# Performance work log

Measured on AMD Instinct MI355X. Metric: run time of the kernel, lower is better.

Reference implementation:

```python
import jax, jax.numpy as jnp
import numpy as np

N_HEAD = 16

def _rope_cos_sin(T, head_dim, dtype):
    # inv_freq over even indices, freqs [T, head_dim//2]
    inv_freq = 1.0 / (10000.0 ** (jnp.arange(0, head_dim, 2, dtype=jnp.float32) / head_dim))
    t = jnp.arange(T, dtype=jnp.float32)
    freqs = t[:, None] * inv_freq[None, :]
    cos = jnp.cos(freqs).astype(dtype)[None, :, None, :]  # [1,T,1,hd/2]
    sin = jnp.sin(freqs).astype(dtype)[None, :, None, :]
    return cos, sin

def _apply_rope(x, cos, sin):
    # x: [B,T,H,hd]; interleaved halves as in the torch module
    x1, x2 = x[..., ::2], x[..., 1::2]
    return jnp.concatenate([x1 * cos - x2 * sin, x1 * sin + x2 * cos], axis=-1)

def setup_inputs() -> dict:
    key = jax.random.key(0)
    k1, k2, k3 = jax.random.split(key, 3)
    B, T, C = 2, 2048, 1024
    x = jax.random.normal(k1, (B, T, C), dtype=jnp.float32)
    # causal mask (mask==0 positions get -inf), broadcast over B and heads
    attn_mask = jnp.tril(jnp.ones((T, T), dtype=bool))[None, None, :, :]
    w_qkv = jax.random.normal(k2, (C, 3 * C), dtype=jnp.float32) * (1.0 / np.sqrt(C))
    w_out = jax.random.normal(k3, (C, C), dtype=jnp.float32) * (1.0 / np.sqrt(C))
    return {"x": x, "attn_mask": attn_mask, "w_qkv": w_qkv, "w_out": w_out}

def reference(x, attn_mask, w_qkv, w_out):
    B, T, C = x.shape
    H = N_HEAD
    hd = C // H
    qkv = x @ w_qkv  # [B,T,3C]
    q, k, v = jnp.split(qkv, 3, axis=2)
    q = q.reshape(B, T, H, hd)
    k = k.reshape(B, T, H, hd)
    v = v.reshape(B, T, H, hd)
    cos, sin = _rope_cos_sin(T, hd, x.dtype)
    q = _apply_rope(q, cos, sin)
    k = _apply_rope(k, cos, sin)
    scale = 1.0 / np.sqrt(hd).astype(np.float32)
    att = jnp.einsum('bthd,bshd->bhts', q, k) * scale  # [B,H,T,T]
    att = jnp.where(attn_mask, att, -jnp.inf)
    att = jax.nn.softmax(att, axis=-1)
    out = jnp.einsum('bhts,bshd->bthd', att, v).reshape(B, T, C)
    out = out @ w_out
    k_t = jnp.transpose(k, (0, 2, 1, 3))  # [B,H,T,hd]
    v_t = jnp.transpose(v, (0, 2, 1, 3))
    return out, k_t, v_t
```

## Files before the change

kernel.cpp:

```cpp
#include <hip/hip_runtime.h>

#define T_SEQ 2048
#define NH    16
#define HD    64
#define CDIM  1024
#define BDIM  2

using floatx4 = __attribute__((ext_vector_type(4))) float;
using bf16x8  = __attribute__((ext_vector_type(8))) __bf16;
using half4   = __attribute__((ext_vector_type(4))) _Float16;
using half8   = __attribute__((ext_vector_type(8))) _Float16;
typedef unsigned short u16;

__device__ __forceinline__ u16 f2bf(float f) {
  unsigned int u = __float_as_uint(f);
  u += 0x7fffu + ((u >> 16) & 1u);
  return (u16)(u >> 16);
}
__device__ __forceinline__ float bf2f(u16 h) {
  return __uint_as_float(((unsigned int)h) << 16);
}
__device__ __forceinline__ u16 f2h(float f) {
  union { _Float16 h; u16 u; } c; c.h = (_Float16)f; return c.u;
}
__device__ __forceinline__ unsigned pk2h(float a, float b) {
  return __builtin_bit_cast(unsigned, __builtin_amdgcn_cvt_pkrtz(a, b));
}
__device__ __forceinline__ void gld16(const void* g, const void* l) {
  __builtin_amdgcn_global_load_lds(
      (const __attribute__((address_space(1))) unsigned int*)(unsigned long long)g,
      (__attribute__((address_space(3))) unsigned int*)(unsigned int)(unsigned long long)l,
      16, 0, 0);
}

__global__ __launch_bounds__(256) void preproc(const float* __restrict__ x,
                                               const float* __restrict__ w_qkv,
                                               const float* __restrict__ w_out,
                                               u16* __restrict__ xb,
                                               u16* __restrict__ wqT,
                                               u16* __restrict__ woT) {
  __shared__ float tile[32][33];
  int blk = blockIdx.x, tid = threadIdx.x;
  if (blk < 4096) {
    int i = blk * 256 + tid;
    float4 v = ((const float4*)x)[i];
    ushort4 o;
    o.x = f2bf(v.x); o.y = f2bf(v.y); o.z = f2bf(v.z); o.w = f2bf(v.w);
    ((ushort4*)xb)[i] = o;
    return;
  }
  const float* W; u16* WT; int K, N, bx, by;
  if (blk < 4096 + 3072) {
    int idx = blk - 4096; W = w_qkv; WT = wqT; K = 1024; N = 3072;
    bx = idx % 96; by = idx / 96;
  } else {
    int idx = blk - 7168; W = w_out; WT = woT; K = 1024; N = 1024;
    bx = idx & 31; by = idx >> 5;
  }
  int n0 = bx * 32, k0 = by * 32;
  int tx = tid & 31, ty = tid >> 5;
#pragma unroll
  for (int i = 0; i < 32; i += 8)
    tile[ty + i][tx] = W[(size_t)(k0 + ty + i) * N + n0 + tx];
  __syncthreads();
#pragma unroll
  for (int i = 0; i < 32; i += 8)
    WT[(size_t)(n0 + ty + i) * K + k0 + tx] = f2bf(tile[tx][ty + i]);
}

template <bool OUT_F32>
__global__ __launch_bounds__(256) void gemm_bt(const u16* __restrict__ A,
                                               const u16* __restrict__ BT,
                                               float* __restrict__ Cf,
                                               u16* __restrict__ Cb,
                                               int M, int N, int K) {
  __shared__ u16 As[128 * 32];
  __shared__ u16 Bs[128 * 32];
  const int tid  = threadIdx.x;
  const int lane = tid & 63, wave = tid >> 6;
  const int quad = lane >> 4, l16 = lane & 15;
  const int wm = (wave & 1) * 64, wn = (wave >> 1) * 64;
  const int row0 = blockIdx.x * 128, col0 = blockIdx.y * 128;
  const int srow = tid >> 2;
  const int sc   = tid & 3;
  const int sgc  = (sc ^ ((srow >> 1) & 3)) * 8;
  floatx4 acc[4][4] = {};
  for (int k0 = 0; k0 < K; k0 += 32) {
    __syncthreads();
    gld16(A  + (size_t)(row0 + srow     ) * K + k0 + sgc, &As[srow * 32 + sc * 8]);
    gld16(A  + (size_t)(row0 + srow + 64) * K + k0 + sgc, &As[(srow + 64) * 32 + sc * 8]);
    gld16(BT + (size_t)(col0 + srow     ) * K + k0 + sgc, &Bs[srow * 32 + sc * 8]);
    gld16(BT + (size_t)(col0 + srow + 64) * K + k0 + sgc, &Bs[(srow + 64) * 32 + sc * 8]);
    __syncthreads();
    bf16x8 af[4], bfv[4];
#pragma unroll
    for (int mt = 0; mt < 4; mt++) {
      int r = wm + mt * 16 + l16;
      af[mt] = *(const bf16x8*)&As[r * 32 + (quad ^ ((r >> 1) & 3)) * 8];
    }
#pragma unroll
    for (int nt = 0; nt < 4; nt++) {
      int r = wn + nt * 16 + l16;
      bfv[nt] = *(const bf16x8*)&Bs[r * 32 + (quad ^ ((r >> 1) & 3)) * 8];
    }
#pragma unroll
    for (int mt = 0; mt < 4; mt++)
#pragma unroll
      for (int nt = 0; nt < 4; nt++)
        acc[mt][nt] = __builtin_amdgcn_mfma_f32_16x16x32_bf16(af[mt], bfv[nt], acc[mt][nt], 0, 0, 0);
  }
#pragma unroll
  for (int mt = 0; mt < 4; mt++)
#pragma unroll
    for (int nt = 0; nt < 4; nt++)
#pragma unroll
      for (int r = 0; r < 4; r++) {
        int row = row0 + wm + mt * 16 + quad * 4 + r;
        int col = col0 + wn + nt * 16 + l16;
        float v = acc[mt][nt][r];
        if (OUT_F32) Cf[(size_t)row * N + col] = v;
        else         Cb[(size_t)row * N + col] = f2bf(v);
      }
}

__global__ __launch_bounds__(256) void rope_vpack(const u16* __restrict__ qkv,
                                                  u16* __restrict__ qf16,
                                                  u16* __restrict__ kf16,
                                                  float* __restrict__ kt_out,
                                                  float* __restrict__ vt_out,
                                                  u16* __restrict__ vtf) {
  int blk = blockIdx.x;
  if (blk < 16384) {
    int gid = blk * 4 + (threadIdx.x >> 6);
    int d   = threadIdx.x & 63;
    int t   = gid & (T_SEQ - 1);
    int h   = (gid >> 11) & 15;
    int b   = gid >> 15;
    const u16* qrow = qkv + ((size_t)(b * T_SEQ + t)) * 3072 + h * 64;
    int i = d & 31;
    unsigned int qp = *(const unsigned int*)(qrow + 2 * i);
    unsigned int kp = *(const unsigned int*)(qrow + 1024 + 2 * i);
    float q1 = bf2f((u16)qp), q2 = bf2f((u16)(qp >> 16));
    float k1 = bf2f((u16)kp), k2 = bf2f((u16)(kp >> 16));
    float inv = expf((float)i * -0.28782313662425572f);
    float ang = (float)t * inv;
    float sn = sinf(ang), cs = cosf(ang);
    float qv = (d < 32) ? (q1 * cs - q2 * sn) : (q1 * sn + q2 * cs);
    float kv = (d < 32) ? (k1 * cs - k2 * sn) : (k1 * sn + k2 * cs);
    size_t o = (size_t)gid * 64 + d;
    qf16[o] = f2h(qv * 0.18033688011112042f);
    kf16[o] = f2h(kv);
    kt_out[o] = kv;
    return;
  }
  __shared__ float tile[64][65];
  int b2 = blk - 16384;
  int t0 = (b2 & 31) * 64;
  int bh = b2 >> 5;
  int b = bh >> 4, h = bh & 15;
  int tx = threadIdx.x & 63, ty = threadIdx.x >> 6;
#pragma unroll
  for (int i = ty; i < 64; i += 4) {
    float v = bf2f(qkv[((size_t)(b * T_SEQ + t0 + i)) * 3072 + 2048 + h * 64 + tx]);
    tile[i][tx] = v;
    vt_out[((size_t)bh * T_SEQ + t0 + i) * 64 + tx] = v;
  }
  __syncthreads();
#pragma unroll
  for (int i = ty; i < 64; i += 4)
    vtf[((size_t)bh * 64 + i) * T_SEQ + t0 + tx] = f2h(tile[tx][i]);
}

__device__ __forceinline__ void qk_dual(const u16* Ks, const half8* qfA, const half8* qfB,
                                        floatx4 (&sA)[8], floatx4 (&sB)[8],
                                        int quad, int l16) {
#pragma unroll
  for (int kc = 0; kc < 2; kc++)
#pragma unroll
    for (int st = 0; st < 8; st++) {
      int srow = st * 16 + l16;
      half8 ak = *(const half8*)&Ks[srow * 64 + (((kc * 4 + quad) ^ (srow & 7)) * 8)];
      sA[st] = __builtin_amdgcn_mfma_f32_16x16x32_f16(ak, qfA[kc], sA[st], 0, 0, 0);
      sB[st] = __builtin_amdgcn_mfma_f32_16x16x32_f16(ak, qfB[kc], sB[st], 0, 0, 0);
    }
}
__device__ __forceinline__ void qk_single(const u16* Ks, const half8* qfA,
                                          floatx4 (&sA)[8], int quad, int l16) {
#pragma unroll
  for (int kc = 0; kc < 2; kc++)
#pragma unroll
    for (int st = 0; st < 8; st++) {
      int srow = st * 16 + l16;
      half8 ak = *(const half8*)&Ks[srow * 64 + (((kc * 4 + quad) ^ (srow & 7)) * 8)];
      sA[st] = __builtin_amdgcn_mfma_f32_16x16x32_f16(ak, qfA[kc], sA[st], 0, 0, 0);
    }
}
__device__ __forceinline__ void apply_mask(floatx4 (&s)[8], int kt, int tw, int quad, int l16) {
  int tg = tw + l16;
#pragma unroll
  for (int st = 0; st < 8; st++) {
    int sg = kt * 128 + st * 16 + quad * 4;
#pragma unroll
    for (int r = 0; r < 4; r++)
      if (sg + r > tg) s[st][r] = -1e30f;
  }
}
__device__ __forceinline__ void softmax_update(floatx4 (&s)[8], float& mrow, float& lrow,
                                               floatx4 (&oacc)[4]) {
  floatx4 vm = s[0];
#pragma unroll
  for (int st = 1; st < 8; st++) {
    vm[0] = fmaxf(vm[0], s[st][0]); vm[1] = fmaxf(vm[1], s[st][1]);
    vm[2] = fmaxf(vm[2], s[st][2]); vm[3] = fmaxf(vm[3], s[st][3]);
  }
  float mx = fmaxf(fmaxf(vm[0], vm[1]), fmaxf(vm[2], vm[3]));
  mx = fmaxf(mx, __shfl_xor(mx, 16));
  mx = fmaxf(mx, __shfl_xor(mx, 32));
  if (!__all(mx <= mrow + 8.f)) {
    float mnew = fmaxf(mrow, mx);
    float alpha = exp2f(mrow - mnew);
    mrow = mnew;
    lrow *= alpha;
#pragma unroll
    for (int dt = 0; dt < 4; dt++) oacc[dt] *= alpha;
  }
  floatx4 vs = {0.f, 0.f, 0.f, 0.f};
#pragma unroll
  for (int st = 0; st < 8; st++) {
#pragma unroll
    for (int r = 0; r < 4; r++) s[st][r] = exp2f(s[st][r] - mrow);
    vs += s[st];
  }
  float rs = (vs[0] + vs[1]) + (vs[2] + vs[3]);
  rs += __shfl_xor(rs, 16);
  rs += __shfl_xor(rs, 32);
  lrow += rs;
}
__device__ __forceinline__ void pv_dual(const u16* Vts, const floatx4 (&sA)[8],
                                        const floatx4 (&sB)[8], floatx4 (&oA)[4],
                                        floatx4 (&oB)[4], int qh2, int ql2, int l16) {
#pragma unroll
  for (int st = 0; st < 8; st++) {
    union { unsigned u[2]; half4 h; } pa, pb;
    pa.u[0] = pk2h(sA[st][0], sA[st][1]); pa.u[1] = pk2h(sA[st][2], sA[st][3]);
    pb.u[0] = pk2h(sB[st][0], sB[st][1]); pb.u[1] = pk2h(sB[st][2], sB[st][3]);
#pragma unroll
    for (int dt = 0; dt < 4; dt++) {
      int drow = dt * 16 + l16;
      half4 av = *(const half4*)&Vts[drow * 128 + (((st * 2 + qh2) ^ (drow & 15)) * 8) + ql2];
      oA[dt] = __builtin_amdgcn_mfma_f32_16x16x16f16(av, pa.h, oA[dt], 0, 0, 0);
      oB[dt] = __builtin_amdgcn_mfma_f32_16x16x16f16(av, pb.h, oB[dt], 0, 0, 0);
    }
  }
}
__device__ __forceinline__ void pv_single(const u16* Vts, const floatx4 (&sA)[8],
                                          floatx4 (&oA)[4], int qh2, int ql2, int l16) {
#pragma unroll
  for (int st = 0; st < 8; st++) {
    union { unsigned u[2]; half4 h; } pa;
    pa.u[0] = pk2h(sA[st][0], sA[st][1]); pa.u[1] = pk2h(sA[st][2], sA[st][3]);
#pragma unroll
    for (int dt = 0; dt < 4; dt++) {
      int drow = dt * 16 + l16;
      half4 av = *(const half4*)&Vts[drow * 128 + (((st * 2 + qh2) ^ (drow & 15)) * 8) + ql2];
      oA[dt] = __builtin_amdgcn_mfma_f32_16x16x16f16(av, pa.h, oA[dt], 0, 0, 0);
    }
  }
}
__device__ __forceinline__ void epilogue(u16* __restrict__ Ob, const floatx4 (&oacc)[4],
                                         float lrow, int b, int h, int tw, int quad, int l16) {
  int t = tw + l16;
  float invl = 1.f / lrow;
#pragma unroll
  for (int dt = 0; dt < 4; dt++) {
    int d0 = dt * 16 + quad * 4;
    ushort4 o;
    o.x = f2bf(oacc[dt][0] * invl);
    o.y = f2bf(oacc[dt][1] * invl);
    o.z = f2bf(oacc[dt][2] * invl);
    o.w = f2bf(oacc[dt][3] * invl);
    *(ushort4*)&Ob[((size_t)(b * T_SEQ) + t) * CDIM + h * HD + d0] = o;
  }
}

__global__ __launch_bounds__(256, 2) void attn_fused(const u16* __restrict__ qf16,
                                                     const u16* __restrict__ kf16,
                                                     const u16* __restrict__ vtf,
                                                     u16* __restrict__ Ob) {
  __shared__ u16 Ks[128 * 64];
  __shared__ u16 Vts[64 * 128];
  const int tid = threadIdx.x;
  const int lane = tid & 63, wave = tid >> 6;
  const int quad = lane >> 4, l16 = lane & 15;
  const int qh2 = quad >> 1, ql2 = (quad & 1) * 4;
  const int j   = blockIdx.x >> 5;
  const int bh  = blockIdx.x & 31;
  const int b = bh >> 4, h = bh & 15;

  const int qtA = 31 - j, qtB = j;
  const int twA = qtA * 64 + wave * 16;
  const int twB = qtB * 64 + wave * 16;
  const int nktA = (qtA >> 1) + 1;
  const int nktB = (qtB >> 1) + 1;

  const u16* QgA = qf16 + ((size_t)bh * T_SEQ + twA) * HD;
  const u16* QgB = qf16 + ((size_t)bh * T_SEQ + twB) * HD;
  half8 qfA[2], qfB[2];
#pragma unroll
  for (int kc = 0; kc < 2; kc++) {
    qfA[kc] = *(const half8*)&QgA[(size_t)l16 * HD + kc * 32 + quad * 8];
    qfB[kc] = *(const half8*)&QgB[(size_t)l16 * HD + kc * 32 + quad * 8];
  }

  floatx4 oaccA[4] = {}, oaccB[4] = {};
  float mA = -1e30f, lA = 0.f;
  float mB = -1e30f, lB = 0.f;

#pragma unroll 1
  for (int kt = 0; kt < nktA; kt++) {
    __syncthreads();
    const size_t koff = ((size_t)bh * T_SEQ + kt * 128) * HD;
    const u16* Vg = vtf + (size_t)bh * HD * T_SEQ + kt * 128;
#pragma unroll
    for (int jj = 0; jj < 4; jj++) {
      int t2 = jj * 256 + tid;
      int r = t2 >> 3, c = t2 & 7;
      gld16(kf16 + koff + r * HD + (c ^ (r & 7)) * 8, &Ks[t2 * 8]);
    }
#pragma unroll
    for (int jj = 0; jj < 4; jj++) {
      int t2 = jj * 256 + tid;
      int r = t2 >> 4, c = t2 & 15;
      gld16(Vg + (size_t)r * T_SEQ + (c ^ (r & 15)) * 8, &Vts[t2 * 8]);
    }
    __syncthreads();

    if (kt < nktB) {
      floatx4 sA[8] = {}, sB[8] = {};
      qk_dual(Ks, qfA, qfB, sA, sB, quad, l16);
      if (kt == nktB - 1) apply_mask(sB, kt, twB, quad, l16);
      softmax_update(sA, mA, lA, oaccA);
      softmax_update(sB, mB, lB, oaccB);
      pv_dual(Vts, sA, sB, oaccA, oaccB, qh2, ql2, l16);
    } else {
      floatx4 sA[8] = {};
      qk_single(Ks, qfA, sA, quad, l16);
      if (kt == nktA - 1) apply_mask(sA, kt, twA, quad, l16);
      softmax_update(sA, mA, lA, oaccA);
      pv_single(Vts, sA, oaccA, qh2, ql2, l16);
    }
  }
  epilogue(Ob, oaccA, lA, b, h, twA, quad, l16);
  epilogue(Ob, oaccB, lB, b, h, twB, quad, l16);
}

extern "C" void kernel_launch(void* const* d_in, const int* in_sizes, int n_in,
                              void* d_out, int out_size, void* d_ws, size_t ws_size,
                              hipStream_t stream) {
  const float* x     = (const float*)d_in[0];
  const float* w_qkv = (const float*)d_in[2];
  const float* w_out = (const float*)d_in[3];
  float* out    = (float*)d_out;
  float* kt_out = out + (size_t)BDIM * T_SEQ * CDIM;
  float* vt_out = kt_out + (size_t)BDIM * T_SEQ * CDIM;

  const size_t F = (size_t)4194304;
  char* base = (char*)d_ws;
  u16* xb   = (u16*)base;
  u16* wqT  = xb + F;
  u16* woT  = wqT + (size_t)3145728;
  u16* qkvb = woT + (size_t)1048576;
  u16* qf16 = qkvb + (size_t)3 * F;
  u16* kf16 = qf16 + F;
  u16* vtf  = (u16*)base;
  u16* Ob   = kf16 + F;

  preproc<<<8192, 256, 0, stream>>>(x, w_qkv, w_out, xb, wqT, woT);
  gemm_bt<false><<<dim3(32, 24), 256, 0, stream>>>(xb, wqT, (float*)nullptr, qkvb, 4096, 3072, 1024);
  rope_vpack<<<17408, 256, 0, stream>>>(qkvb, qf16, kf16, kt_out, vt_out, vtf);
  attn_fused<<<512, 256, 0, stream>>>(qf16, kf16, vtf, Ob);
  gemm_bt<true><<<dim3(32, 8), 256, 0, stream>>>(Ob, woT, out, (u16*)nullptr, 4096, 1024, 1024);
}
```

Measured before the change: 215.3 us.

## Double-buffer LDS tiles in GEMM and attention to overlap loads with MFMA

Both the bf16 GEMM and the fused attention kernel now use two LDS buffers. The next K/V or A/B tile is prefetched with direct global-to-LDS loads while the current tile is consumed, and partial vmcnt waits plus raw barriers replace the full __syncthreads pairs. The attention kernel also raises wave priority around its MFMA sections with s_setprio. This doubles LDS use, which may reduce occupancy (the attention kernel now needs 64 KB per block at launch bounds of 2 blocks per CU). Correctness depends on the hand-counted vmcnt values matching the number of outstanding loads.

```diff
diff --git a/kernel.cpp b/kernel.cpp
--- a/kernel.cpp
+++ b/kernel.cpp
@@ -74,8 +74,8 @@
                                                float* __restrict__ Cf,
                                                u16* __restrict__ Cb,
                                                int M, int N, int K) {
-  __shared__ u16 As[128 * 32];
-  __shared__ u16 Bs[128 * 32];
+  __shared__ u16 As[2][128 * 32];
+  __shared__ u16 Bs[2][128 * 32];
   const int tid  = threadIdx.x;
   const int lane = tid & 63, wave = tid >> 6;
   const int quad = lane >> 4, l16 = lane & 15;
@@ -85,23 +85,33 @@
   const int sc   = tid & 3;
   const int sgc  = (sc ^ ((srow >> 1) & 3)) * 8;
   floatx4 acc[4][4] = {};
-  for (int k0 = 0; k0 < K; k0 += 32) {
-    __syncthreads();
-    gld16(A  + (size_t)(row0 + srow     ) * K + k0 + sgc, &As[srow * 32 + sc * 8]);
-    gld16(A  + (size_t)(row0 + srow + 64) * K + k0 + sgc, &As[(srow + 64) * 32 + sc * 8]);
-    gld16(BT + (size_t)(col0 + srow     ) * K + k0 + sgc, &Bs[srow * 32 + sc * 8]);
-    gld16(BT + (size_t)(col0 + srow + 64) * K + k0 + sgc, &Bs[(srow + 64) * 32 + sc * 8]);
-    __syncthreads();
+
+  auto stage = [&](int buf, int k0) {
+    gld16(A  + (size_t)(row0 + srow     ) * K + k0 + sgc, &As[buf][srow * 32 + sc * 8]);
+    gld16(A  + (size_t)(row0 + srow + 64) * K + k0 + sgc, &As[buf][(srow + 64) * 32 + sc * 8]);
+    gld16(BT + (size_t)(col0 + srow     ) * K + k0 + sgc, &Bs[buf][srow * 32 + sc * 8]);
+    gld16(BT + (size_t)(col0 + srow + 64) * K + k0 + sgc, &Bs[buf][(srow + 64) * 32 + sc * 8]);
+  };
+
+  const int nk = K >> 5;
+  stage(0, 0);
+  for (int ki = 0; ki < nk; ki++) {
+    const int cur = ki & 1;
+    __builtin_amdgcn_s_barrier();
+    int kn = ki + 1 < nk ? ki + 1 : nk - 1;
+    stage(cur ^ 1, kn << 5);
+    asm volatile("s_waitcnt vmcnt(4)" ::: "memory");
+    __builtin_amdgcn_s_barrier();
     bf16x8 af[4], bfv[4];
 #pragma unroll
     for (int mt = 0; mt < 4; mt++) {
       int r = wm + mt * 16 + l16;
-      af[mt] = *(const bf16x8*)&As[r * 32 + (quad ^ ((r >> 1) & 3)) * 8];
+      af[mt] = *(const bf16x8*)&As[cur][r * 32 + (quad ^ ((r >> 1) & 3)) * 8];
     }
 #pragma unroll
     for (int nt = 0; nt < 4; nt++) {
       int r = wn + nt * 16 + l16;
-      bfv[nt] = *(const bf16x8*)&Bs[r * 32 + (quad ^ ((r >> 1) & 3)) * 8];
+      bfv[nt] = *(const bf16x8*)&Bs[cur][r * 32 + (quad ^ ((r >> 1) & 3)) * 8];
     }
 #pragma unroll
     for (int mt = 0; mt < 4; mt++)
@@ -109,6 +119,7 @@
       for (int nt = 0; nt < 4; nt++)
         acc[mt][nt] = __builtin_amdgcn_mfma_f32_16x16x32_bf16(af[mt], bfv[nt], acc[mt][nt], 0, 0, 0);
   }
+  asm volatile("s_waitcnt vmcnt(0)" ::: "memory");
 #pragma unroll
   for (int mt = 0; mt < 4; mt++)
 #pragma unroll
@@ -287,8 +298,8 @@
                                                      const u16* __restrict__ kf16,
                                                      const u16* __restrict__ vtf,
                                                      u16* __restrict__ Ob) {
-  __shared__ u16 Ks[128 * 64];
-  __shared__ u16 Vts[64 * 128];
+  __shared__ u16 Ks[2][128 * 64];
+  __shared__ u16 Vts[2][64 * 128];
   const int tid = threadIdx.x;
   const int lane = tid & 63, wave = tid >> 6;
   const int quad = lane >> 4, l16 = lane & 15;
@@ -312,44 +323,65 @@
     qfB[kc] = *(const half8*)&QgB[(size_t)l16 * HD + kc * 32 + quad * 8];
   }
 
+  auto stage = [&](int buf, int kt) {
+    const size_t koff = ((size_t)bh * T_SEQ + kt * 128) * HD;
+    const u16* Vg = vtf + (size_t)bh * HD * T_SEQ + kt * 128;
+    u16* Kd = &Ks[buf][0];
+    u16* Vd = &Vts[buf][0];
+#pragma unroll
+    for (int jj = 0; jj < 4; jj++) {
+      int t2 = jj * 256 + tid;
+      int r = t2 >> 3, c = t2 & 7;
+      gld16(kf16 + koff + r * HD + (c ^ (r & 7)) * 8, Kd + t2 * 8);
+    }
+#pragma unroll
+    for (int jj = 0; jj < 4; jj++) {
+      int t2 = jj * 256 + tid;
+      int r = t2 >> 4, c = t2 & 15;
+      gld16(Vg + (size_t)r * T_SEQ + (c ^ (r & 15)) * 8, Vd + t2 * 8);
+    }
+  };
+
   floatx4 oaccA[4] = {}, oaccB[4] = {};
   float mA = -1e30f, lA = 0.f;
   float mB = -1e30f, lB = 0.f;
 
+  stage(0, 0);
 #pragma unroll 1
   for (int kt = 0; kt < nktA; kt++) {
-    __syncthreads();
-    const size_t koff = ((size_t)bh * T_SEQ + kt * 128) * HD;
-    const u16* Vg = vtf + (size_t)bh * HD * T_SEQ + kt * 128;
-#pragma unroll
-    for (int jj = 0; jj < 4; jj++) {
-      int t2 = jj * 256 + tid;
-      int r = t2 >> 3, c = t2 & 7;
-      gld16(kf16 + koff + r * HD + (c ^ (r & 7)) * 8, &Ks[t2 * 8]);
-    }
-#pragma unroll
-    for (int jj = 0; jj < 4; jj++) {
-      int t2 = jj * 256 + tid;
-      int r = t2 >> 4, c = t2 & 15;
-      gld16(Vg + (size_t)r * T_SEQ + (c ^ (r & 15)) * 8, &Vts[t2 * 8]);
-    }
-    __syncthreads();
+    const int cur = kt & 1;
+    __builtin_amdgcn_s_barrier();
+    int ktn = kt + 1 < nktA ? kt + 1 : nktA - 1;
+    stage(cur ^ 1, ktn);
+    asm volatile("s_waitcnt vmcnt(8)" ::: "memory");
+    __builtin_amdgcn_s_barrier();
+    const u16* Kc = &Ks[cur][0];
+    const u16* Vc = &Vts[cur][0];
 
     if (kt < nktB) {
       floatx4 sA[8] = {}, sB[8] = {};
-      qk_dual(Ks, qfA, qfB, sA, sB, quad, l16);
+      __builtin_amdgcn_s_setprio(1);
+      qk_dual(Kc, qfA, qfB, sA, sB, quad, l16);
+      __builtin_amdgcn_s_setprio(0);
       if (kt == nktB - 1) apply_mask(sB, kt, twB, quad, l16);
       softmax_update(sA, mA, lA, oaccA);
       softmax_update(sB, mB, lB, oaccB);
-      pv_dual(Vts, sA, sB, oaccA, oaccB, qh2, ql2, l16);
+      __builtin_amdgcn_s_setprio(1);
+      pv_dual(Vc, sA, sB, oaccA, oaccB, qh2, ql2, l16);
+      __builtin_amdgcn_s_setprio(0);
     } else {
       floatx4 sA[8] = {};
-      qk_single(Ks, qfA, sA, quad, l16);
+      __builtin_amdgcn_s_setprio(1);
+      qk_single(Kc, qfA, sA, quad, l16);
+      __builtin_amdgcn_s_setprio(0);
       if (kt == nktA - 1) apply_mask(sA, kt, twA, quad, l16);
       softmax_update(sA, mA, lA, oaccA);
-      pv_single(Vts, sA, oaccA, qh2, ql2, l16);
-    }
-  }
+      __builtin_amdgcn_s_setprio(1);
+      pv_single(Vc, sA, oaccA, qh2, ql2, l16);
+      __builtin_amdgcn_s_setprio(0);
+    }
+  }
+  asm volatile("s_waitcnt vmcnt(0)" ::: "memory");
   epilogue(Ob, oaccA, lA, b, h, twA, quad, l16);
   epilogue(Ob, oaccB, lB, b, h, twB, quad, l16);
 }
```

Result: faster. 210.7 us (-2.2%).
